# Optimization experiments

Hardware: AMD Instinct MI355X
Metric: run time of the kernel (lower is better)

Reference implementation:

```python
import jax, jax.numpy as jnp
import numpy as np

NEG_SLOPE = 0.01  # torch leaky_relu default

def _lrelu(x):
    return jax.nn.leaky_relu(x, NEG_SLOPE)

def _l2norm(x, axis):
    # torch F.normalize(p=2, eps=1e-12)
    n = jnp.linalg.norm(x, axis=axis, keepdims=True)
    return x / jnp.maximum(n, 1e-12)

def setup_inputs() -> dict:
    key = jax.random.key(0)
    ks = jax.random.split(key, 12)
    Nda, Nq, C, Din, Dout = 10000, 64, 1024, 128, 256
    target_adj = (jax.random.uniform(ks[0], (Nda, Nda)) < 0.002).astype(jnp.float32)
    query_adj = (jax.random.uniform(ks[1], (Nq, Nq)) < 0.2).astype(jnp.float32)
    node_features_da = jax.random.normal(ks[2], (Nda, Din), dtype=jnp.float32)
    node_features_q = jax.random.normal(ks[3], (Nq, Din), dtype=jnp.float32)
    candidate_set = jax.random.randint(ks[4], (C,), 0, Nda)
    candidate_adj = (jax.random.uniform(ks[5], (C, C)) < 0.01).astype(jnp.float32)
    s_in = 1.0 / np.sqrt(Din).astype(np.float32)
    s_out = 1.0 / np.sqrt(Dout).astype(np.float32)
    W1_da = jax.random.normal(ks[6], (Din, Dout), dtype=jnp.float32) * s_in
    W1_q = jax.random.normal(ks[7], (Din, Dout), dtype=jnp.float32) * s_in
    W2_da = jax.random.normal(ks[8], (Dout, Dout), dtype=jnp.float32) * s_out
    W2_q = jax.random.normal(ks[9], (Dout, Dout), dtype=jnp.float32) * s_out
    threshold = jnp.float32(0.2)
    return {"target_adj": target_adj, "node_features_da": node_features_da,
            "query_adj": query_adj, "node_features_q": node_features_q,
            "candidate_set": candidate_set, "candidate_adj": candidate_adj,
            "threshold": threshold, "W1_da": W1_da, "W1_q": W1_q,
            "W2_da": W2_da, "W2_q": W2_q}

def _cross_cosine(q, da, candidate_set):
    # cosine similarity between each query node and each candidate target node: [Nq, C]
    return _l2norm(q, 1) @ _l2norm(da[candidate_set], 1).T

def reference(target_adj, node_features_da, query_adj, node_features_q,
              candidate_set, candidate_adj, threshold, W1_da, W1_q, W2_da, W2_q):
    # layer 1: GCN propagation on both graphs (gcn(adj,x) = adj @ x @ W)
    da1 = _lrelu(target_adj @ (node_features_da @ W1_da))   # [Nda, D]
    q1 = _lrelu(query_adj @ (node_features_q @ W1_q))       # [Nq, D]
    c1 = _cross_cosine(q1, da1, candidate_set)               # [Nq, C]
    pre_da1 = da1[candidate_set]                             # [C, D]
    # NOTE: da1[candidate_set].data = ... mutates a temporary in torch -> no-op on da1
    att_da1 = _lrelu(da1)                                    # dropout in eval = identity
    h1_q = c1 @ pre_da1                                      # [Nq, D]
    att_q1 = _lrelu(q1 + _l2norm(h1_q, 0))
    # layer 2
    da2 = _lrelu(target_adj @ (att_da1 @ W2_da))
    q2 = _lrelu(query_adj @ (att_q1 @ W2_q))
    c2 = _cross_cosine(q2, da2, candidate_set)
    pre_da2 = da2[candidate_set]
    att_da2 = _lrelu(da2)                                    # in-place update is again a no-op
    h2_q = c2 @ pre_da2
    att_q2 = _lrelu(q2 + _l2norm(h2_q, 0))
    # graph-level matching score per target node
    emb = jnp.mean(att_q2, axis=0, keepdims=True)            # [1, D]
    num = att_da2 @ emb[0]                                   # [Nda]
    den = jnp.maximum(jnp.linalg.norm(att_da2, axis=1) * jnp.linalg.norm(emb), 1e-8)
    end = (num / den)[None, :]                               # [1, Nda]
    # threshold selection expressed with a mask (jit-safe, same math: excluded
    # rows/cols are zero and do not affect L2 norms, sums, or the trace)
    m = (end[0] > threshold).astype(att_da2.dtype)           # [Nda]
    F_ = att_da2 * m[:, None]
    re_adj = F_ @ F_.T                                       # [Nda, Nda]
    nor_re = _l2norm(re_adj, 1) * target_adj                 # elementwise with original adj
    cnt = jnp.sum(m)
    total = jnp.sum(nor_re)
    tr = jnp.trace(nor_re)
    has = cnt > 0
    pre_avg_degree = jnp.where(has, total / jnp.maximum(cnt, 1.0), 0.0)
    pre_avg_nodes = jnp.where(has, tr, 0.0)
    pre_density = jnp.where(has, 2.0 * total / (tr * (tr - 1.0) + 1e-4), 0.0)
    return (end, att_da2, att_q2, pre_avg_degree, pre_density, pre_avg_nodes)
```

## Files before the change

kernel.cpp:

```cpp
#include <hip/hip_runtime.h>
#include <hip/hip_bf16.h>

constexpr int NDA = 10000;
constexpr int NQ  = 64;
constexpr int CND = 1024;
constexpr int DIN = 128;
constexpr int D   = 256;
constexpr int CAP = 96;

#define LRELU(x) ((x) >= 0.f ? (x) : 0.01f * (x))

typedef __attribute__((ext_vector_type(8))) short short8;
typedef __attribute__((ext_vector_type(4))) float f32x4;

__device__ __forceinline__ float wave_red64(float v) {
#pragma unroll
    for (int o = 32; o; o >>= 1) v += __shfl_down(v, o);
    return v;
}

__global__ __launch_bounds__(256) void build_csr(const float* __restrict__ adj,
                                                 int* __restrict__ cols,
                                                 int* __restrict__ rowcnt) {
    int row = blockIdx.x;
    __shared__ int scnt;
    if (threadIdx.x == 0) scnt = 0;
    __syncthreads();
    const float4* rp = (const float4*)(adj + (size_t)row * NDA);
    for (int i = threadIdx.x; i < NDA / 4; i += 256) {
        float4 v = rp[i];
        if (v.x != 0.f) { int s = atomicAdd(&scnt, 1); if (s < CAP) cols[row * CAP + s] = 4 * i; }
        if (v.y != 0.f) { int s = atomicAdd(&scnt, 1); if (s < CAP) cols[row * CAP + s] = 4 * i + 1; }
        if (v.z != 0.f) { int s = atomicAdd(&scnt, 1); if (s < CAP) cols[row * CAP + s] = 4 * i + 2; }
        if (v.w != 0.f) { int s = atomicAdd(&scnt, 1); if (s < CAP) cols[row * CAP + s] = 4 * i + 3; }
    }
    __syncthreads();
    if (threadIdx.x == 0) rowcnt[row] = min(scnt, CAP);
}

template <int W>
__global__ void spmm_f32(const int* __restrict__ cols,
                         const int* __restrict__ rowcnt,
                         const float* __restrict__ X,
                         __hip_bfloat16* __restrict__ out) {
    int row = blockIdx.x;
    int d = threadIdx.x;
    int cnt = rowcnt[row];
    __shared__ int sc[CAP];
    if (d < CAP && d < cnt) sc[d] = cols[row * CAP + d];
    __syncthreads();
    float a0 = 0.f, a1 = 0.f, a2 = 0.f, a3 = 0.f;
    int k = 0;
    for (; k + 4 <= cnt; k += 4) {
        a0 += X[(size_t)sc[k + 0] * W + d];
        a1 += X[(size_t)sc[k + 1] * W + d];
        a2 += X[(size_t)sc[k + 2] * W + d];
        a3 += X[(size_t)sc[k + 3] * W + d];
    }
    for (; k < cnt; k++) a0 += X[(size_t)sc[k] * W + d];
    out[(size_t)row * W + d] = __float2bfloat16((a0 + a1) + (a2 + a3));
}

__global__ void spmm_bf16(const int* __restrict__ cols,
                          const int* __restrict__ rowcnt,
                          const __hip_bfloat16* __restrict__ X,
                          __hip_bfloat16* __restrict__ out) {
    int row = blockIdx.x;
    int d = threadIdx.x;
    int cnt = rowcnt[row];
    __shared__ int sc[CAP];
    if (d < CAP && d < cnt) sc[d] = cols[row * CAP + d];
    __syncthreads();
    float a0 = 0.f, a1 = 0.f, a2 = 0.f, a3 = 0.f;
    int k = 0;
    for (; k + 4 <= cnt; k += 4) {
        a0 += __bfloat162float(X[(size_t)sc[k + 0] * D + d]);
        a1 += __bfloat162float(X[(size_t)sc[k + 1] * D + d]);
        a2 += __bfloat162float(X[(size_t)sc[k + 2] * D + d]);
        a3 += __bfloat162float(X[(size_t)sc[k + 3] * D + d]);
    }
    for (; k < cnt; k++) a0 += __bfloat162float(X[(size_t)sc[k] * D + d]);
    out[(size_t)row * D + d] = __float2bfloat16((a0 + a1) + (a2 + a3));
}

template <int KDIM, int EPI>
__global__ __launch_bounds__(256) void mfma_gemm(const __hip_bfloat16* __restrict__ A,
                                                 const float* __restrict__ B,
                                                 float* __restrict__ C,
                                                 float* __restrict__ C2,
                                                 __hip_bfloat16* __restrict__ bfout,
                                                 float* __restrict__ rowsq,
                                                 int M) {
    __shared__ __hip_bfloat16 Al[64][56];
    __shared__ __hip_bfloat16 Bl[64][56];
    const int bm = blockIdx.x * 64;
    const int bn = blockIdx.y * 64;
    const int tid = threadIdx.x;
    const int wave = tid >> 6, lane = tid & 63;
    const int quad = lane >> 4, l16 = lane & 15;
    f32x4 acc[4] = {};
    for (int k0 = 0; k0 < KDIM; k0 += 32) {
        {
            int m = tid >> 2;
            int koff = (tid & 3) * 8;
            uint4 v = make_uint4(0, 0, 0, 0);
            if (bm + m < M) v = *(const uint4*)(A + (size_t)(bm + m) * KDIM + k0 + koff);
            *(uint4*)(&Al[m][koff]) = v;
        }
        {
            int nl = tid >> 2;
            int kb = (tid & 3) * 8;
            __hip_bfloat16 tmp[8];
#pragma unroll
            for (int u = 0; u < 8; u++)
                tmp[u] = __float2bfloat16(B[(size_t)(k0 + kb + u) * D + bn + nl]);
            *(uint4*)(&Bl[nl][kb]) = *(const uint4*)tmp;
        }
        __syncthreads();
        short8 af = *(const short8*)(&Al[wave * 16 + l16][quad * 8]);
#pragma unroll
        for (int ns = 0; ns < 4; ns++) {
            short8 bf = *(const short8*)(&Bl[ns * 16 + l16][quad * 8]);
            acc[ns] = __builtin_amdgcn_mfma_f32_16x16x32_bf16(af, bf, acc[ns], 0, 0, 0);
        }
        __syncthreads();
    }
    float rp[4] = {};
#pragma unroll
    for (int ns = 0; ns < 4; ns++) {
        int col = bn + ns * 16 + l16;
#pragma unroll
        for (int reg = 0; reg < 4; reg++) {
            int r = bm + wave * 16 + quad * 4 + reg;
            if (r < M) {
                float v = acc[ns][reg];
                if (EPI == 0) {
                    C[(size_t)r * D + col] = v;
                } else {
                    float da = LRELU(v);
                    C[(size_t)r * D + col] = da;
                    rp[reg] += da * da;
                    float att = LRELU(da);
                    if (EPI == 2) C2[(size_t)r * D + col] = att;
                    bfout[(size_t)r * D + col] = __float2bfloat16(att);
                }
            }
        }
    }
    if (EPI != 0) {
#pragma unroll
        for (int reg = 0; reg < 4; reg++) {
            int r = bm + wave * 16 + quad * 4 + reg;
            if (r < M && rp[reg] != 0.f) atomicAdd(&rowsq[r], rp[reg]);
        }
    }
}

template <bool GATHER>
__global__ __launch_bounds__(256) void ata_mfma(const float* __restrict__ A,
                                                const int* __restrict__ cand,
                                                const float* __restrict__ scale,
                                                float* __restrict__ Out,
                                                int nrc) {
    __shared__ __hip_bfloat16 SAl[64][56];
    __shared__ __hip_bfloat16 SBl[64][56];
    __shared__ int sidx[512];
    __shared__ float sscl[512];
    const int ti = blockIdx.x, tj = blockIdx.y;
    const int base = blockIdx.z * nrc;
    const int tid = threadIdx.x;
    const int wave = tid >> 6, lane = tid & 63;
    const int quad = lane >> 4, l16 = lane & 15;
    for (int i = tid; i < nrc; i += 256) {
        int g = base + i;
        if (GATHER) {
            int ri = cand[g];
            sidx[i] = ri;
            sscl[i] = 1.f / fmaxf(sqrtf(scale[ri]), 1e-12f);
        } else {
            if (g < NDA) { sidx[i] = g; sscl[i] = scale[g]; }
            else         { sidx[i] = -1; sscl[i] = 0.f; }
        }
    }
    __syncthreads();
    f32x4 acc[4] = {};
    for (int kc = 0; kc < nrc; kc += 32) {
        {
            int c = tid >> 2;
            int kb = (tid & 3) * 8;
            __hip_bfloat16 ta[8], tb[8];
#pragma unroll
            for (int u = 0; u < 8; u++) {
                int ri = sidx[kc + kb + u];
                float av = 0.f, bv = 0.f;
                if (ri >= 0) {
                    av = A[(size_t)ri * D + ti * 64 + c] * sscl[kc + kb + u];
                    bv = A[(size_t)ri * D + tj * 64 + c];
                }
                ta[u] = __float2bfloat16(av);
                tb[u] = __float2bfloat16(bv);
            }
            *(uint4*)(&SAl[c][kb]) = *(const uint4*)ta;
            *(uint4*)(&SBl[c][kb]) = *(const uint4*)tb;
        }
        __syncthreads();
        short8 af = *(const short8*)(&SAl[wave * 16 + l16][quad * 8]);
#pragma unroll
        for (int ns = 0; ns < 4; ns++) {
            short8 bf = *(const short8*)(&SBl[ns * 16 + l16][quad * 8]);
            acc[ns] = __builtin_amdgcn_mfma_f32_16x16x32_bf16(af, bf, acc[ns], 0, 0, 0);
        }
        __syncthreads();
    }
#pragma unroll
    for (int ns = 0; ns < 4; ns++) {
        int col = tj * 64 + ns * 16 + l16;
#pragma unroll
        for (int reg = 0; reg < 4; reg++) {
            int row = ti * 64 + wave * 16 + quad * 4 + reg;
            float v = acc[ns][reg];
            if (v != 0.f) atomicAdd(&Out[(size_t)row * D + col], v);
        }
    }
}

__global__ __launch_bounds__(256) void qpath_kernel(const float* __restrict__ Fq,
                                                    const float* __restrict__ Wq,
                                                    const float* __restrict__ Qadj,
                                                    float* __restrict__ q_out,
                                                    float* __restrict__ rnqsq,
                                                    int K) {
    __shared__ float As[16][68];
    __shared__ float Bs[16][68];
    __shared__ float Xs[64][68];
    __shared__ float Qs[64][68];
    __shared__ float sq[64];
    const int bn = blockIdx.x * 64;
    const int tid = threadIdx.x;
    const int tx = tid & 15, ty = tid >> 4;
    float acc[4][4] = {};
    for (int k0 = 0; k0 < K; k0 += 16) {
        {
            int m = tid >> 2;
            int k4 = (tid & 3) * 4;
            float4 v = *(const float4*)(Fq + (size_t)m * K + k0 + k4);
            As[k4 + 0][m] = v.x; As[k4 + 1][m] = v.y; As[k4 + 2][m] = v.z; As[k4 + 3][m] = v.w;
        }
        {
            int kk = tid >> 4;
            int n4 = (tid & 15) * 4;
            float4 v = *(const float4*)(Wq + (size_t)(k0 + kk) * D + bn + n4);
            Bs[kk][n4 + 0] = v.x; Bs[kk][n4 + 1] = v.y; Bs[kk][n4 + 2] = v.z; Bs[kk][n4 + 3] = v.w;
        }
        __syncthreads();
#pragma unroll
        for (int kk = 0; kk < 16; kk++) {
            float av[4], bv[4];
#pragma unroll
            for (int i = 0; i < 4; i++) av[i] = As[kk][ty * 4 + i];
#pragma unroll
            for (int j = 0; j < 4; j++) bv[j] = Bs[kk][tx * 4 + j];
#pragma unroll
            for (int i = 0; i < 4; i++)
#pragma unroll
                for (int j = 0; j < 4; j++) acc[i][j] += av[i] * bv[j];
        }
        __syncthreads();
    }
#pragma unroll
    for (int i = 0; i < 4; i++)
#pragma unroll
        for (int j = 0; j < 4; j++) Xs[ty * 4 + i][tx * 4 + j] = acc[i][j];
    for (int l = tid; l < NQ * NQ; l += 256) Qs[l >> 6][l & 63] = Qadj[l];
    if (tid < 64) sq[tid] = 0.f;
    __syncthreads();
    float a2[4][4] = {};
#pragma unroll 4
    for (int kk = 0; kk < NQ; kk++) {
        float av[4], bv[4];
#pragma unroll
        for (int i = 0; i < 4; i++) av[i] = Qs[ty * 4 + i][kk];
#pragma unroll
        for (int j = 0; j < 4; j++) bv[j] = Xs[kk][tx * 4 + j];
#pragma unroll
        for (int i = 0; i < 4; i++)
#pragma unroll
            for (int j = 0; j < 4; j++) a2[i][j] += av[i] * bv[j];
    }
#pragma unroll
    for (int i = 0; i < 4; i++) {
        float rp = 0.f;
#pragma unroll
        for (int j = 0; j < 4; j++) {
            float v = LRELU(a2[i][j]);
            q_out[(ty * 4 + i) * D + bn + tx * 4 + j] = v;
            rp += v * v;
        }
        atomicAdd(&sq[ty * 4 + i], rp);
    }
    __syncthreads();
    if (tid < 64) atomicAdd(&rnqsq[tid], sq[tid]);
}

template <bool EMB>
__global__ __launch_bounds__(256) void hq_attq_kernel(const float* __restrict__ q,
                                                      const float* __restrict__ rnqsq,
                                                      float* __restrict__ M,
                                                      float* __restrict__ attq,
                                                      float* __restrict__ emb) {
    __shared__ float As[16][68];
    __shared__ float Bs[16][68];
    __shared__ float cred[16][64];
    __shared__ float sinv[64];
    const int bn = blockIdx.x * 64;
    const int tid = threadIdx.x;
    const int tx = tid & 15, ty = tid >> 4;
    const int am = tid >> 2;
    const float ascale = 1.f / fmaxf(sqrtf(rnqsq[am]), 1e-12f);
    float acc[4][4] = {};
    const float4 z4 = make_float4(0.f, 0.f, 0.f, 0.f);
    for (int k0 = 0; k0 < D; k0 += 16) {
        {
            int k4 = (tid & 3) * 4;
            float4 v = *(const float4*)(q + (size_t)am * D + k0 + k4);
            As[k4 + 0][am] = v.x * ascale; As[k4 + 1][am] = v.y * ascale;
            As[k4 + 2][am] = v.z * ascale; As[k4 + 3][am] = v.w * ascale;
        }
        {
            int kk = tid >> 4;
            int n4 = (tid & 15) * 4;
            float4 v = *(const float4*)(M + (size_t)(k0 + kk) * D + bn + n4);
            *(float4*)(M + (size_t)(k0 + kk) * D + bn + n4) = z4;
            Bs[kk][n4 + 0] = v.x; Bs[kk][n4 + 1] = v.y; Bs[kk][n4 + 2] = v.z; Bs[kk][n4 + 3] = v.w;
        }
        __syncthreads();
#pragma unroll
        for (int kk = 0; kk < 16; kk++) {
            float av[4], bv[4];
#pragma unroll
            for (int i = 0; i < 4; i++) av[i] = As[kk][ty * 4 + i];
#pragma unroll
            for (int j = 0; j < 4; j++) bv[j] = Bs[kk][tx * 4 + j];
#pragma unroll
            for (int i = 0; i < 4; i++)
#pragma unroll
                for (int j = 0; j < 4; j++) acc[i][j] += av[i] * bv[j];
        }
        __syncthreads();
    }
#pragma unroll
    for (int j = 0; j < 4; j++) {
        float p = 0.f;
#pragma unroll
        for (int i = 0; i < 4; i++) p += acc[i][j] * acc[i][j];
        cred[ty][tx * 4 + j] = p;
    }
    __syncthreads();
    if (tid < 64) {
        float s = 0.f;
#pragma unroll
        for (int t = 0; t < 16; t++) s += cred[t][tid];
        sinv[tid] = 1.f / fmaxf(sqrtf(s), 1e-12f);
    }
    __syncthreads();
    float esum[4] = {};
#pragma unroll
    for (int i = 0; i < 4; i++) {
        int r = ty * 4 + i;
        float4 q4 = *(const float4*)(q + (size_t)r * D + bn + tx * 4);
        float4 v;
        v.x = LRELU(q4.x + acc[i][0] * sinv[tx * 4 + 0]);
        v.y = LRELU(q4.y + acc[i][1] * sinv[tx * 4 + 1]);
        v.z = LRELU(q4.z + acc[i][2] * sinv[tx * 4 + 2]);
        v.w = LRELU(q4.w + acc[i][3] * sinv[tx * 4 + 3]);
        *(float4*)(attq + (size_t)r * D + bn + tx * 4) = v;
        if (EMB) { esum[0] += v.x; esum[1] += v.y; esum[2] += v.z; esum[3] += v.w; }
    }
    if (EMB) {
        __syncthreads();
#pragma unroll
        for (int j = 0; j < 4; j++) cred[ty][tx * 4 + j] = esum[j];
        __syncthreads();
        if (tid < 64) {
            float s = 0.f;
#pragma unroll
            for (int t = 0; t < 16; t++) s += cred[t][tid];
            emb[bn + tid] = s * (1.f / (float)NQ);
        }
    }
}

__global__ __launch_bounds__(256) void end_kernel(const float* __restrict__ A,
                                                  const float* __restrict__ emb,
                                                  const float* __restrict__ thr_p,
                                                  float* __restrict__ endv,
                                                  float* __restrict__ m,
                                                  float* __restrict__ cnt) {
    __shared__ float se[D];
    __shared__ float red[4];
    __shared__ float scnt, sembn;
    int d = threadIdx.x;
    se[d] = emb[d];
    if (d == 0) scnt = 0.f;
    __syncthreads();
    int w = d >> 6, lane = d & 63;
    {
        float p = wave_red64(se[d] * se[d]);
        if (lane == 0) red[w] = p;
    }
    __syncthreads();
    if (d == 0) sembn = sqrtf(red[0] + red[1] + red[2] + red[3]);
    __syncthreads();
    float embn = sembn;
    float thr = *thr_p;
    int row = blockIdx.x * 4 + w;
    const float* ar = A + (size_t)row * D;
    float num = 0.f, sq = 0.f;
#pragma unroll
    for (int s = 0; s < 4; s++) {
        float v = ar[lane + 64 * s];
        num += v * se[lane + 64 * s];
        sq += v * v;
    }
#pragma unroll
    for (int o = 32; o; o >>= 1) { num += __shfl_down(num, o); sq += __shfl_down(sq, o); }
    if (lane == 0) {
        float den = fmaxf(sqrtf(sq) * embn, 1e-8f);
        float e = num / den;
        endv[row] = e;
        float mv = e > thr ? 1.f : 0.f;
        m[row] = mv;
        if (mv != 0.f) atomicAdd(&scnt, 1.f);
    }
    __syncthreads();
    if (d == 0 && scnt != 0.f) atomicAdd(cnt, scnt);
}

__global__ __launch_bounds__(256) void final_kernel(const int* __restrict__ cols,
                                                    const int* __restrict__ rowcnt,
                                                    const float* __restrict__ m,
                                                    const float* __restrict__ A,
                                                    const float* __restrict__ H,
                                                    double* __restrict__ total,
                                                    double* __restrict__ tr) {
    int i = blockIdx.x;
    if (m[i] == 0.f) return;
    __shared__ float sa[D];
    __shared__ int sc[CAP];
    __shared__ float red[4], red2[4];
    __shared__ float sdenom;
    int d = threadIdx.x;
    float av = A[(size_t)i * D + d];
    sa[d] = av;
    int cnt = rowcnt[i];
    if (d < cnt) sc[d] = cols[i * CAP + d];
    float p = wave_red64(av * H[(size_t)i * D + d]);
    int w = d >> 6, lane = d & 63;
    if (lane == 0) red[w] = p;
    __syncthreads();
    if (d == 0) sdenom = fmaxf(sqrtf(red[0] + red[1] + red[2] + red[3]), 1e-12f);
    __syncthreads();
    float accs = 0.f, acct = 0.f;
    for (int k = w; k < cnt; k += 4) {
        int j = sc[k];
        if (m[j] != 0.f) {
            const float* aj = A + (size_t)j * D;
            float t = sa[lane] * aj[lane] + sa[lane + 64] * aj[lane + 64]
                    + sa[lane + 128] * aj[lane + 128] + sa[lane + 192] * aj[lane + 192];
            t = wave_red64(t);
            if (lane == 0) { accs += t; if (j == i) acct += t; }
        }
    }
    if (lane == 0) { red[w] = accs; red2[w] = acct; }
    __syncthreads();
    if (d == 0) {
        float s = red[0] + red[1] + red[2] + red[3];
        float t2 = red2[0] + red2[1] + red2[2] + red2[3];
        double inv = 1.0 / (double)sdenom;
        if (s != 0.f) atomicAdd(total, (double)s * inv);
        if (t2 != 0.f) atomicAdd(tr, (double)t2 * inv);
    }
}

__global__ void scalars_kernel(const float* __restrict__ cnt,
                               const double* __restrict__ total,
                               const double* __restrict__ tr,
                               float* __restrict__ out) {
    float c = *cnt;
    float T = (float)*total;
    float R = (float)*tr;
    bool has = c > 0.f;
    out[0] = has ? (T / fmaxf(c, 1.f)) : 0.f;
    out[1] = has ? (2.f * T / (R * (R - 1.f) + 1e-4f)) : 0.f;
    out[2] = has ? R : 0.f;
}

extern "C" void kernel_launch(void* const* d_in, const int* in_sizes, int n_in,
                              void* d_out, int out_size, void* d_ws, size_t ws_size,
                              hipStream_t stream) {
    (void)in_sizes; (void)n_in; (void)out_size; (void)ws_size;
    const float* adj  = (const float*)d_in[0];
    const float* Fda  = (const float*)d_in[1];
    const float* Qadj = (const float*)d_in[2];
    const float* Fq   = (const float*)d_in[3];
    const int*   cand = (const int*)d_in[4];
    const float* thr  = (const float*)d_in[6];
    const float* W1da = (const float*)d_in[7];
    const float* W1q  = (const float*)d_in[8];
    const float* W2da = (const float*)d_in[9];
    const float* W2q  = (const float*)d_in[10];

    float* out = (float*)d_out;
    float* o_end    = out;
    float* o_attda2 = out + NDA;
    float* o_attq2  = out + NDA + (size_t)NDA * D;
    float* o_sc     = o_attq2 + NQ * D;

    char* w = (char*)d_ws;
    size_t off = 0;
    auto alloc = [&](size_t b) { size_t r = off; off += (b + 255) & ~(size_t)255; return r; };
    float* bufB = (float*)(w + alloc((size_t)NDA * D * 4));
    float* bufC = (float*)(w + alloc((size_t)NDA * D * 4));
    __hip_bfloat16* S1bf      = (__hip_bfloat16*)(w + alloc((size_t)NDA * DIN * 2));
    __hip_bfloat16* Tbf       = (__hip_bfloat16*)(w + alloc((size_t)NDA * D * 2));
    __hip_bfloat16* attda1_bf = (__hip_bfloat16*)(w + alloc((size_t)NDA * D * 2));
    __hip_bfloat16* attda2_bf = (__hip_bfloat16*)(w + alloc((size_t)NDA * D * 2));
    int* colsb   = (int*)(w + alloc((size_t)NDA * CAP * 4));
    int* rowcntb = (int*)(w + alloc((size_t)NDA * 4));
    float* mbuf  = (float*)(w + alloc((size_t)NDA * 4));
    size_t zsz = 262144 * 2 + 160000 * 2 + 256 * 2 + 64;
    char* zbase = w + alloc(zsz);
    float* Gb      = (float*)zbase;
    float* Mb      = (float*)(zbase + 262144);
    float* rsq1    = (float*)(zbase + 524288);
    float* rsq2    = (float*)(zbase + 524288 + 160000);
    float* rnqsq1  = (float*)(zbase + 524288 + 320000);
    float* rnqsq2  = (float*)(zbase + 524288 + 320256);
    float* cntb    = (float*)(zbase + 524288 + 320512);
    double* totb   = (double*)(zbase + 524288 + 320520);
    double* trb    = (double*)(zbase + 524288 + 320528);
    float* q1b  = (float*)(w + alloc((size_t)NQ * D * 4));
    float* aq1  = (float*)(w + alloc((size_t)NQ * D * 4));
    float* q2b  = (float*)(w + alloc((size_t)NQ * D * 4));
    float* embb = (float*)(w + alloc((size_t)D * 4));

    hipMemsetAsync(zbase, 0, zsz, stream);

    const dim3 gMM((NDA + 63) / 64, D / 64);

    build_csr<<<NDA, 256, 0, stream>>>(adj, colsb, rowcntb);
    qpath_kernel<<<D / 64, 256, 0, stream>>>(Fq, W1q, Qadj, q1b, rnqsq1, DIN);
    spmm_f32<DIN><<<NDA, DIN, 0, stream>>>(colsb, rowcntb, Fda, S1bf);
    mfma_gemm<DIN, 1><<<gMM, 256, 0, stream>>>(S1bf, W1da, bufB, nullptr,
                                               attda1_bf, rsq1, NDA);
    ata_mfma<true><<<dim3(4, 4, 4), 256, 0, stream>>>(bufB, cand, rsq1, Mb, 256);
    hq_attq_kernel<false><<<D / 64, 256, 0, stream>>>(q1b, rnqsq1, Mb, aq1, nullptr);
    qpath_kernel<<<D / 64, 256, 0, stream>>>(aq1, W2q, Qadj, q2b, rnqsq2, D);
    spmm_bf16<<<NDA, D, 0, stream>>>(colsb, rowcntb, attda1_bf, Tbf);
    mfma_gemm<D, 2><<<gMM, 256, 0, stream>>>(Tbf, W2da, bufC, o_attda2,
                                             attda2_bf, rsq2, NDA);
    ata_mfma<true><<<dim3(4, 4, 4), 256, 0, stream>>>(bufC, cand, rsq2, Mb, 256);
    hq_attq_kernel<true><<<D / 64, 256, 0, stream>>>(q2b, rnqsq2, Mb, o_attq2, embb);
    end_kernel<<<NDA / 4, 256, 0, stream>>>(o_attda2, embb, thr, o_end, mbuf, cntb);
    ata_mfma<false><<<dim3(4, 4, 20), 256, 0, stream>>>(o_attda2, nullptr, mbuf, Gb, 512);
    mfma_gemm<D, 0><<<gMM, 256, 0, stream>>>(attda2_bf, Gb, bufB, nullptr,
                                             nullptr, nullptr, NDA);
    final_kernel<<<NDA, 256, 0, stream>>>(colsb, rowcntb, mbuf, o_attda2, bufB, totb, trb);
    scalars_kernel<<<1, 1, 0, stream>>>(cntb, totb, trb, o_sc);
}
```

Baseline: 1.046 ms.

## Fuse CSR build with first gather, gather into GEMM2, scalars into final

The adjacency scan now also does the first sparse aggregation of the input features, reusing the column list held in shared memory instead of launching a separate SpMM. The second sparse aggregation is done inside the second GEMM's prologue, which loads gathered rows straight into LDS and drops the intermediate Tbf buffer and one launch. The scalar-output kernel is folded into final_kernel with a last-block-done atomic counter. In exchange, each of the four column-tile blocks in GEMM2 repeats the same row gather, and the gather runs on only one block's worth of waves before the MFMA loop starts.

```diff
diff --git a/kernel.cpp b/kernel.cpp
--- a/kernel.cpp
+++ b/kernel.cpp
@@ -13,81 +13,55 @@
 typedef __attribute__((ext_vector_type(8))) short short8;
 typedef __attribute__((ext_vector_type(4))) float f32x4;
 
+struct alignas(8) bf16x4 { __hip_bfloat16 h[4]; };
+
 __device__ __forceinline__ float wave_red64(float v) {
 #pragma unroll
     for (int o = 32; o; o >>= 1) v += __shfl_down(v, o);
     return v;
 }
 
-__global__ __launch_bounds__(256) void build_csr(const float* __restrict__ adj,
-                                                 int* __restrict__ cols,
-                                                 int* __restrict__ rowcnt) {
+__global__ __launch_bounds__(256) void build_gather(const float* __restrict__ adj,
+                                                    const float* __restrict__ Fda,
+                                                    int* __restrict__ cols,
+                                                    int* __restrict__ rowcnt,
+                                                    __hip_bfloat16* __restrict__ S1bf) {
     int row = blockIdx.x;
+    __shared__ int sc[CAP];
     __shared__ int scnt;
     if (threadIdx.x == 0) scnt = 0;
     __syncthreads();
     const float4* rp = (const float4*)(adj + (size_t)row * NDA);
     for (int i = threadIdx.x; i < NDA / 4; i += 256) {
         float4 v = rp[i];
-        if (v.x != 0.f) { int s = atomicAdd(&scnt, 1); if (s < CAP) cols[row * CAP + s] = 4 * i; }
-        if (v.y != 0.f) { int s = atomicAdd(&scnt, 1); if (s < CAP) cols[row * CAP + s] = 4 * i + 1; }
-        if (v.z != 0.f) { int s = atomicAdd(&scnt, 1); if (s < CAP) cols[row * CAP + s] = 4 * i + 2; }
-        if (v.w != 0.f) { int s = atomicAdd(&scnt, 1); if (s < CAP) cols[row * CAP + s] = 4 * i + 3; }
-    }
-    __syncthreads();
-    if (threadIdx.x == 0) rowcnt[row] = min(scnt, CAP);
-}
-
-template <int W>
-__global__ void spmm_f32(const int* __restrict__ cols,
-                         const int* __restrict__ rowcnt,
-                         const float* __restrict__ X,
-                         __hip_bfloat16* __restrict__ out) {
-    int row = blockIdx.x;
-    int d = threadIdx.x;
-    int cnt = rowcnt[row];
-    __shared__ int sc[CAP];
-    if (d < CAP && d < cnt) sc[d] = cols[row * CAP + d];
-    __syncthreads();
-    float a0 = 0.f, a1 = 0.f, a2 = 0.f, a3 = 0.f;
-    int k = 0;
-    for (; k + 4 <= cnt; k += 4) {
-        a0 += X[(size_t)sc[k + 0] * W + d];
-        a1 += X[(size_t)sc[k + 1] * W + d];
-        a2 += X[(size_t)sc[k + 2] * W + d];
-        a3 += X[(size_t)sc[k + 3] * W + d];
-    }
-    for (; k < cnt; k++) a0 += X[(size_t)sc[k] * W + d];
-    out[(size_t)row * W + d] = __float2bfloat16((a0 + a1) + (a2 + a3));
-}
-
-__global__ void spmm_bf16(const int* __restrict__ cols,
-                          const int* __restrict__ rowcnt,
-                          const __hip_bfloat16* __restrict__ X,
-                          __hip_bfloat16* __restrict__ out) {
-    int row = blockIdx.x;
-    int d = threadIdx.x;
-    int cnt = rowcnt[row];
-    __shared__ int sc[CAP];
-    if (d < CAP && d < cnt) sc[d] = cols[row * CAP + d];
-    __syncthreads();
-    float a0 = 0.f, a1 = 0.f, a2 = 0.f, a3 = 0.f;
-    int k = 0;
-    for (; k + 4 <= cnt; k += 4) {
-        a0 += __bfloat162float(X[(size_t)sc[k + 0] * D + d]);
-        a1 += __bfloat162float(X[(size_t)sc[k + 1] * D + d]);
-        a2 += __bfloat162float(X[(size_t)sc[k + 2] * D + d]);
-        a3 += __bfloat162float(X[(size_t)sc[k + 3] * D + d]);
-    }
-    for (; k < cnt; k++) a0 += __bfloat162float(X[(size_t)sc[k] * D + d]);
-    out[(size_t)row * D + d] = __float2bfloat16((a0 + a1) + (a2 + a3));
+        if (v.x != 0.f) { int s = atomicAdd(&scnt, 1); if (s < CAP) sc[s] = 4 * i; }
+        if (v.y != 0.f) { int s = atomicAdd(&scnt, 1); if (s < CAP) sc[s] = 4 * i + 1; }
+        if (v.z != 0.f) { int s = atomicAdd(&scnt, 1); if (s < CAP) sc[s] = 4 * i + 2; }
+        if (v.w != 0.f) { int s = atomicAdd(&scnt, 1); if (s < CAP) sc[s] = 4 * i + 3; }
+    }
+    __syncthreads();
+    int cnt = min(scnt, CAP);
+    if (threadIdx.x == 0) rowcnt[row] = cnt;
+    for (int k = threadIdx.x; k < cnt; k += 256) cols[row * CAP + k] = sc[k];
+    if (threadIdx.x < DIN) {
+        int d = threadIdx.x;
+        float a0 = 0.f, a1 = 0.f, a2 = 0.f, a3 = 0.f;
+        int k = 0;
+        for (; k + 4 <= cnt; k += 4) {
+            a0 += Fda[(size_t)sc[k + 0] * DIN + d];
+            a1 += Fda[(size_t)sc[k + 1] * DIN + d];
+            a2 += Fda[(size_t)sc[k + 2] * DIN + d];
+            a3 += Fda[(size_t)sc[k + 3] * DIN + d];
+        }
+        for (; k < cnt; k++) a0 += Fda[(size_t)sc[k] * DIN + d];
+        S1bf[(size_t)row * DIN + d] = __float2bfloat16((a0 + a1) + (a2 + a3));
+    }
 }
 
 template <int KDIM, int EPI>
 __global__ __launch_bounds__(256) void mfma_gemm(const __hip_bfloat16* __restrict__ A,
                                                  const float* __restrict__ B,
                                                  float* __restrict__ C,
-                                                 float* __restrict__ C2,
                                                  __hip_bfloat16* __restrict__ bfout,
                                                  float* __restrict__ rowsq,
                                                  int M) {
@@ -140,9 +114,7 @@
                     float da = LRELU(v);
                     C[(size_t)r * D + col] = da;
                     rp[reg] += da * da;
-                    float att = LRELU(da);
-                    if (EPI == 2) C2[(size_t)r * D + col] = att;
-                    bfout[(size_t)r * D + col] = __float2bfloat16(att);
+                    bfout[(size_t)r * D + col] = __float2bfloat16(LRELU(da));
                 }
             }
         }
@@ -153,6 +125,97 @@
             int r = bm + wave * 16 + quad * 4 + reg;
             if (r < M && rp[reg] != 0.f) atomicAdd(&rowsq[r], rp[reg]);
         }
+    }
+}
+
+__global__ __launch_bounds__(256) void gemm2_fused(const int* __restrict__ cols,
+                                                   const int* __restrict__ rowcnt,
+                                                   const __hip_bfloat16* __restrict__ X,
+                                                   const float* __restrict__ B,
+                                                   float* __restrict__ C,
+                                                   float* __restrict__ C2,
+                                                   __hip_bfloat16* __restrict__ bfout,
+                                                   float* __restrict__ rowsq,
+                                                   int M) {
+    constexpr int AST = 264;
+    __shared__ __hip_bfloat16 Al[64][AST];
+    __shared__ __hip_bfloat16 Bl[64][56];
+    const int bm = blockIdx.x * 64;
+    const int bn = blockIdx.y * 64;
+    const int tid = threadIdx.x;
+    const int wave = tid >> 6, lane = tid & 63;
+    const int quad = lane >> 4, l16 = lane & 15;
+    for (int rr = wave; rr < 64; rr += 4) {
+        int row = bm + rr;
+        float a0 = 0.f, a1 = 0.f, a2 = 0.f, a3 = 0.f;
+        if (row < M) {
+            int cnt = rowcnt[row];
+            const int* cp = cols + row * CAP;
+            int k = 0;
+            for (; k + 2 <= cnt; k += 2) {
+                bf16x4 v0 = *(const bf16x4*)(X + (size_t)cp[k] * D + lane * 4);
+                bf16x4 v1 = *(const bf16x4*)(X + (size_t)cp[k + 1] * D + lane * 4);
+                a0 += __bfloat162float(v0.h[0]) + __bfloat162float(v1.h[0]);
+                a1 += __bfloat162float(v0.h[1]) + __bfloat162float(v1.h[1]);
+                a2 += __bfloat162float(v0.h[2]) + __bfloat162float(v1.h[2]);
+                a3 += __bfloat162float(v0.h[3]) + __bfloat162float(v1.h[3]);
+            }
+            if (k < cnt) {
+                bf16x4 v0 = *(const bf16x4*)(X + (size_t)cp[k] * D + lane * 4);
+                a0 += __bfloat162float(v0.h[0]);
+                a1 += __bfloat162float(v0.h[1]);
+                a2 += __bfloat162float(v0.h[2]);
+                a3 += __bfloat162float(v0.h[3]);
+            }
+        }
+        bf16x4 t;
+        t.h[0] = __float2bfloat16(a0); t.h[1] = __float2bfloat16(a1);
+        t.h[2] = __float2bfloat16(a2); t.h[3] = __float2bfloat16(a3);
+        *(bf16x4*)(&Al[rr][lane * 4]) = t;
+    }
+    __syncthreads();
+    f32x4 acc[4] = {};
+    for (int k0 = 0; k0 < D; k0 += 32) {
+        {
+            int nl = tid >> 2;
+            int kb = (tid & 3) * 8;
+            __hip_bfloat16 tmp[8];
+#pragma unroll
+            for (int u = 0; u < 8; u++)
+                tmp[u] = __float2bfloat16(B[(size_t)(k0 + kb + u) * D + bn + nl]);
+            *(uint4*)(&Bl[nl][kb]) = *(const uint4*)tmp;
+        }
+        __syncthreads();
+        short8 af = *(const short8*)(&Al[wave * 16 + l16][k0 + quad * 8]);
+#pragma unroll
+        for (int ns = 0; ns < 4; ns++) {
+            short8 bf = *(const short8*)(&Bl[ns * 16 + l16][quad * 8]);
+            acc[ns] = __builtin_amdgcn_mfma_f32_16x16x32_bf16(af, bf, acc[ns], 0, 0, 0);
+        }
+        __syncthreads();
+    }
+    float rp[4] = {};
+#pragma unroll
+    for (int ns = 0; ns < 4; ns++) {
+        int col = bn + ns * 16 + l16;
+#pragma unroll
+        for (int reg = 0; reg < 4; reg++) {
+            int r = bm + wave * 16 + quad * 4 + reg;
+            if (r < M) {
+                float v = acc[ns][reg];
+                float da = LRELU(v);
+                C[(size_t)r * D + col] = da;
+                rp[reg] += da * da;
+                float att = LRELU(da);
+                C2[(size_t)r * D + col] = att;
+                bfout[(size_t)r * D + col] = __float2bfloat16(att);
+            }
+        }
+    }
+#pragma unroll
+    for (int reg = 0; reg < 4; reg++) {
+        int r = bm + wave * 16 + quad * 4 + reg;
+        if (r < M && rp[reg] != 0.f) atomicAdd(&rowsq[r], rp[reg]);
     }
 }
 
@@ -442,57 +505,62 @@
                                                     const float* __restrict__ A,
                                                     const float* __restrict__ H,
                                                     double* __restrict__ total,
-                                                    double* __restrict__ tr) {
+                                                    double* __restrict__ tr,
+                                                    const float* __restrict__ cntp,
+                                                    int* __restrict__ donecnt,
+                                                    float* __restrict__ osc) {
     int i = blockIdx.x;
-    if (m[i] == 0.f) return;
-    __shared__ float sa[D];
-    __shared__ int sc[CAP];
-    __shared__ float red[4], red2[4];
-    __shared__ float sdenom;
     int d = threadIdx.x;
-    float av = A[(size_t)i * D + d];
-    sa[d] = av;
-    int cnt = rowcnt[i];
-    if (d < cnt) sc[d] = cols[i * CAP + d];
-    float p = wave_red64(av * H[(size_t)i * D + d]);
-    int w = d >> 6, lane = d & 63;
-    if (lane == 0) red[w] = p;
-    __syncthreads();
-    if (d == 0) sdenom = fmaxf(sqrtf(red[0] + red[1] + red[2] + red[3]), 1e-12f);
-    __syncthreads();
-    float accs = 0.f, acct = 0.f;
-    for (int k = w; k < cnt; k += 4) {
-        int j = sc[k];
-        if (m[j] != 0.f) {
-            const float* aj = A + (size_t)j * D;
-            float t = sa[lane] * aj[lane] + sa[lane + 64] * aj[lane + 64]
-                    + sa[lane + 128] * aj[lane + 128] + sa[lane + 192] * aj[lane + 192];
-            t = wave_red64(t);
-            if (lane == 0) { accs += t; if (j == i) acct += t; }
-        }
-    }
-    if (lane == 0) { red[w] = accs; red2[w] = acct; }
-    __syncthreads();
+    if (m[i] != 0.f) {
+        __shared__ float sa[D];
+        __shared__ int sc[CAP];
+        __shared__ float red[4], red2[4];
+        __shared__ float sdenom;
+        float av = A[(size_t)i * D + d];
+        sa[d] = av;
+        int cnt = rowcnt[i];
+        if (d < cnt) sc[d] = cols[i * CAP + d];
+        float p = wave_red64(av * H[(size_t)i * D + d]);
+        int w = d >> 6, lane = d & 63;
+        if (lane == 0) red[w] = p;
+        __syncthreads();
+        if (d == 0) sdenom = fmaxf(sqrtf(red[0] + red[1] + red[2] + red[3]), 1e-12f);
+        __syncthreads();
+        float accs = 0.f, acct = 0.f;
+        for (int k = w; k < cnt; k += 4) {
+            int j = sc[k];
+            if (m[j] != 0.f) {
+                const float* aj = A + (size_t)j * D;
+                float t = sa[lane] * aj[lane] + sa[lane + 64] * aj[lane + 64]
+                        + sa[lane + 128] * aj[lane + 128] + sa[lane + 192] * aj[lane + 192];
+                t = wave_red64(t);
+                if (lane == 0) { accs += t; if (j == i) acct += t; }
+            }
+        }
+        if (lane == 0) { red[w] = accs; red2[w] = acct; }
+        __syncthreads();
+        if (d == 0) {
+            float s = red[0] + red[1] + red[2] + red[3];
+            float t2 = red2[0] + red2[1] + red2[2] + red2[3];
+            double inv = 1.0 / (double)sdenom;
+            if (s != 0.f) atomicAdd(total, (double)s * inv);
+            if (t2 != 0.f) atomicAdd(tr, (double)t2 * inv);
+        }
+    }
     if (d == 0) {
-        float s = red[0] + red[1] + red[2] + red[3];
-        float t2 = red2[0] + red2[1] + red2[2] + red2[3];
-        double inv = 1.0 / (double)sdenom;
-        if (s != 0.f) atomicAdd(total, (double)s * inv);
-        if (t2 != 0.f) atomicAdd(tr, (double)t2 * inv);
-    }
-}
-
-__global__ void scalars_kernel(const float* __restrict__ cnt,
-                               const double* __restrict__ total,
-                               const double* __restrict__ tr,
-                               float* __restrict__ out) {
-    float c = *cnt;
-    float T = (float)*total;
-    float R = (float)*tr;
-    bool has = c > 0.f;
-    out[0] = has ? (T / fmaxf(c, 1.f)) : 0.f;
-    out[1] = has ? (2.f * T / (R * (R - 1.f) + 1e-4f)) : 0.f;
-    out[2] = has ? R : 0.f;
+        __threadfence();
+        int t = atomicAdd(donecnt, 1);
+        if (t == NDA - 1) {
+            float c = *cntp;
+            double T = atomicAdd(total, 0.0);
+            double R = atomicAdd(tr, 0.0);
+            float Tf = (float)T, Rf = (float)R;
+            bool has = c > 0.f;
+            osc[0] = has ? (Tf / fmaxf(c, 1.f)) : 0.f;
+            osc[1] = has ? (2.f * Tf / (Rf * (Rf - 1.f) + 1e-4f)) : 0.f;
+            osc[2] = has ? Rf : 0.f;
+        }
+    }
 }
 
 extern "C" void kernel_launch(void* const* d_in, const int* in_sizes, int n_in,
@@ -522,7 +590,6 @@
     float* bufB = (float*)(w + alloc((size_t)NDA * D * 4));
     float* bufC = (float*)(w + alloc((size_t)NDA * D * 4));
     __hip_bfloat16* S1bf      = (__hip_bfloat16*)(w + alloc((size_t)NDA * DIN * 2));
-    __hip_bfloat16* Tbf       = (__hip_bfloat16*)(w + alloc((size_t)NDA * D * 2));
     __hip_bfloat16* attda1_bf = (__hip_bfloat16*)(w + alloc((size_t)NDA * D * 2));
     __hip_bfloat16* attda2_bf = (__hip_bfloat16*)(w + alloc((size_t)NDA * D * 2));
     int* colsb   = (int*)(w + alloc((size_t)NDA * CAP * 4));
@@ -539,6 +606,7 @@
     float* cntb    = (float*)(zbase + 524288 + 320512);
     double* totb   = (double*)(zbase + 524288 + 320520);
     double* trb    = (double*)(zbase + 524288 + 320528);
+    int* doneb     = (int*)(zbase + 524288 + 320536);
     float* q1b  = (float*)(w + alloc((size_t)NQ * D * 4));
     float* aq1  = (float*)(w + alloc((size_t)NQ * D * 4));
     float* q2b  = (float*)(w + alloc((size_t)NQ * D * 4));
@@ -548,23 +616,19 @@
 
     const dim3 gMM((NDA + 63) / 64, D / 64);
 
-    build_csr<<<NDA, 256, 0, stream>>>(adj, colsb, rowcntb);
+    build_gather<<<NDA, 256, 0, stream>>>(adj, Fda, colsb, rowcntb, S1bf);
     qpath_kernel<<<D / 64, 256, 0, stream>>>(Fq, W1q, Qadj, q1b, rnqsq1, DIN);
-    spmm_f32<DIN><<<NDA, DIN, 0, stream>>>(colsb, rowcntb, Fda, S1bf);
-    mfma_gemm<DIN, 1><<<gMM, 256, 0, stream>>>(S1bf, W1da, bufB, nullptr,
-                                               attda1_bf, rsq1, NDA);
+    mfma_gemm<DIN, 1><<<gMM, 256, 0, stream>>>(S1bf, W1da, bufB, attda1_bf, rsq1, NDA);
     ata_mfma<true><<<dim3(4, 4, 4), 256, 0, stream>>>(bufB, cand, rsq1, Mb, 256);
     hq_attq_kernel<false><<<D / 64, 256, 0, stream>>>(q1b, rnqsq1, Mb, aq1, nullptr);
     qpath_kernel<<<D / 64, 256, 0, stream>>>(aq1, W2q, Qadj, q2b, rnqsq2, D);
-    spmm_bf16<<<NDA, D, 0, stream>>>(colsb, rowcntb, attda1_bf, Tbf);
-    mfma_gemm<D, 2><<<gMM, 256, 0, stream>>>(Tbf, W2da, bufC, o_attda2,
-                                             attda2_bf, rsq2, NDA);
+    gemm2_fused<<<gMM, 256, 0, stream>>>(colsb, rowcntb, attda1_bf, W2da,
+                                         bufC, o_attda2, attda2_bf, rsq2, NDA);
     ata_mfma<true><<<dim3(4, 4, 4), 256, 0, stream>>>(bufC, cand, rsq2, Mb, 256);
     hq_attq_kernel<true><<<D / 64, 256, 0, stream>>>(q2b, rnqsq2, Mb, o_attq2, embb);
     end_kernel<<<NDA / 4, 256, 0, stream>>>(o_attda2, embb, thr, o_end, mbuf, cntb);
     ata_mfma<false><<<dim3(4, 4, 20), 256, 0, stream>>>(o_attda2, nullptr, mbuf, Gb, 512);
-    mfma_gemm<D, 0><<<gMM, 256, 0, stream>>>(attda2_bf, Gb, bufB, nullptr,
-                                             nullptr, nullptr, NDA);
-    final_kernel<<<NDA, 256, 0, stream>>>(colsb, rowcntb, mbuf, o_attda2, bufB, totb, trb);
-    scalars_kernel<<<1, 1, 0, stream>>>(cntb, totb, trb, o_sc);
-}
+    mfma_gemm<D, 0><<<gMM, 256, 0, stream>>>(attda2_bf, Gb, bufB, nullptr, nullptr, NDA);
+    final_kernel<<<NDA, 256, 0, stream>>>(colsb, rowcntb, mbuf, o_attda2, bufB,
+                                          totb, trb, cntb, doneb, o_sc);
+}
```

New measurement: 1.295 ms. 23.9% more time.
